# Optimization experiments

Measured on AMD Instinct MI355X. Metric: run time of the kernel, lower is better.

The kernel has to match this reference:

```python
import jax, jax.numpy as jnp
import numpy as np
from jax import lax

HIST_L = 8
HIST_AB = 64


def _hist2d(x1, nbin=HIST_AB):
    # channels 1 (a) and 2 (b); nonzero-masked weighted 2D histogram over [0,1]x[0,1]
    B = x1.shape[0]
    a = x1[:, 1].reshape(B, -1)
    b = x1[:, 2].reshape(B, -1)
    va = (a + 1.0) * 0.5
    vb = (b + 1.0) * 0.5
    w = ((a != 0) & (b != 0) & (va >= 0) & (va <= 1) & (vb >= 0) & (vb <= 1)).astype(jnp.float32)
    ia = jnp.clip(jnp.floor(va * nbin).astype(jnp.int32), 0, nbin - 1)
    ib = jnp.clip(jnp.floor(vb * nbin).astype(jnp.int32), 0, nbin - 1)
    idx = (jnp.arange(B, dtype=jnp.int32)[:, None] * (nbin * nbin) + ia * nbin + ib).reshape(-1)
    H = jax.ops.segment_sum(w.reshape(-1), idx, num_segments=B * nbin * nbin)
    H = H.reshape(B, nbin, nbin)
    H = H / jnp.sum(H, axis=(1, 2), keepdims=True)
    # np.rot90 followed by np.flip(axis=0) == transpose
    H = jnp.swapaxes(H, 1, 2)
    return H[:, None]  # [B,1,64,64]


def _hist1d(x1, nbin=HIST_L):
    # channel 0 (L); 1D histogram (second dummy dim has a single always-in-range bin)
    B = x1.shape[0]
    l = x1[:, 0].reshape(B, -1)
    v = (l + 1.0) * 0.5
    w = ((l != 0) & (v >= 0) & (v <= 1)).astype(jnp.float32)
    ib = jnp.clip(jnp.floor(v * nbin).astype(jnp.int32), 0, nbin - 1)
    idx = (jnp.arange(B, dtype=jnp.int32)[:, None] * nbin + ib).reshape(-1)
    H = jax.ops.segment_sum(w.reshape(-1), idx, num_segments=B * nbin).reshape(B, nbin)
    H = H / jnp.sum(H, axis=1, keepdims=True)
    return H[:, :, None, None]  # [B,8,1,1]


def _bn(x, g, b, m, v, eps=1e-5):
    inv = g * lax.rsqrt(v + eps)
    return x * inv[None, :, None, None] + (b - m * inv)[None, :, None, None]


def _hen(inp, w1, g1, b1, m1, v1, w2, g2, b2, m2, v2, wl, bl):
    dn = ('NCHW', 'OIHW', 'NCHW')
    # Conv 9->128, k1, pad 1 (grows 64 -> 66, matching torch padding=(1,1))
    y = lax.conv_general_dilated(inp, w1, (1, 1), [(1, 1), (1, 1)], dimension_numbers=dn)
    y = _bn(y, g1, b1, m1, v1)
    # MaxPool k3 s2 p1: 66 -> 33
    y = lax.reduce_window(y, -jnp.inf, lax.max, (1, 1, 3, 3), (1, 1, 2, 2),
                          [(0, 0), (0, 0), (1, 1), (1, 1)])
    y = jax.nn.relu(y)
    # Conv 128->1024, k3, pad 1
    y = lax.conv_general_dilated(y, w2, (1, 1), [(1, 1), (1, 1)], dimension_numbers=dn)
    y = jax.nn.relu(_bn(y, g2, b2, m2, v2))
    y = jnp.mean(y, axis=(2, 3))  # adaptive avg pool (1,1) -> [B,1024]
    return y @ wl.T + bl


def setup_inputs() -> dict:
    key = jax.random.key(0)
    ks = jax.random.split(key, 10)
    B, H, W = 16, 512, 512
    x = jax.random.normal(ks[0], (B, 2048), dtype=jnp.float32)
    x1 = jax.random.uniform(ks[1], (B, 3, H, W), dtype=jnp.float32)  # in [0,1) subset of [-1,1]
    w1 = jax.random.normal(ks[2], (128, 9, 1, 1), dtype=jnp.float32) * 0.1
    w2 = jax.random.normal(ks[3], (1024, 128, 3, 3), dtype=jnp.float32) * 0.02
    wl = jax.random.normal(ks[4], (256, 1024), dtype=jnp.float32) * 0.03
    bl = jax.random.normal(ks[5], (256,), dtype=jnp.float32) * 0.01
    g1 = jnp.ones((128,), jnp.float32); b1 = jnp.zeros((128,), jnp.float32)
    m1 = jnp.zeros((128,), jnp.float32); v1 = jnp.ones((128,), jnp.float32)
    g2 = jnp.ones((1024,), jnp.float32); b2 = jnp.zeros((1024,), jnp.float32)
    m2 = jnp.zeros((1024,), jnp.float32); v2 = jnp.ones((1024,), jnp.float32)
    return {"x": x, "x1": x1, "w1": w1, "g1": g1, "b1": b1, "m1": m1, "v1": v1,
            "w2": w2, "g2": g2, "b2": b2, "m2": m2, "v2": v2, "wl": wl, "bl": bl}


def reference(x, x1, w1, g1, b1, m1, v1, w2, g2, b2, m2, v2, wl, bl):
    hist_ab = _hist2d(x1)                                   # [B,1,64,64]
    hist_l = jnp.broadcast_to(_hist1d(x1), (x1.shape[0], HIST_L, HIST_AB, HIST_AB))
    hist_inp = jnp.concatenate([hist_ab, hist_l], axis=1)   # [B,9,64,64]
    h = _hen(hist_inp, w1, g1, b1, m1, v1, w2, g2, b2, m2, v2, wl, bl)  # [B,256]
    # NIMA.forward returns the concatenated features x (head/softmax output is discarded)
    return jnp.concatenate([x, h], axis=1)                  # [B,2304]
```

## Files before the change

kernel.cpp:

```cpp
#include <hip/hip_runtime.h>
#include <hip/hip_bf16.h>
#include <math.h>

typedef __attribute__((ext_vector_type(8))) short bf16x8;
typedef __attribute__((ext_vector_type(4))) float f32x4;
typedef __attribute__((ext_vector_type(8))) int i32x8;

#define HW 262144
#define M_SP 1089

#define OFF_CNT1P 0
#define OFF_HAB   2048
#define OFF_HL    67584
#define OFF_W2R   68096
#define OFF_ZT    362(0+1008)
#undef OFF_ZT
#define OFF_ZT    363008
#define OFF_FEATP 1026048
#define OFF_PART  1173504

__device__ inline unsigned wred_u32(unsigned v) {
#pragma unroll
    for (int off = 32; off > 0; off >>= 1) v += __shfl_down(v, off);
    return v;
}

__device__ inline unsigned char f2e4m3(float x) {
    unsigned s = (__float_as_uint(x) >> 31) << 7;
    float a = fabsf(x);
    if (a >= 464.f) return (unsigned char)(s | 0x7E);
    if (a < 0.0009765625f) return (unsigned char)s;
    int e; float m = frexpf(a, &e); (void)m;
    int E = e + 6;
    if (E >= 1) {
        float f = ldexpf(a, -(e - 1));
        int q = (int)rintf((f - 1.f) * 8.f);
        if (q == 8) { q = 0; ++E; }
        if (E >= 16) return (unsigned char)(s | 0x7E);
        return (unsigned char)(s | (E << 3) | q);
    } else {
        int q = (int)rintf(ldexpf(a, 9));
        if (q >= 8) return (unsigned char)(s | 0x08);
        return (unsigned char)(s | q);
    }
}

__global__ __launch_bounds__(512) void prep_kernel(const float* __restrict__ x1,
                                                   const float* __restrict__ w2,
                                                   unsigned* __restrict__ part,
                                                   unsigned* __restrict__ cnt1p,
                                                   unsigned char* __restrict__ w2r) {
    const int bid = blockIdx.x;
    const int tid = threadIdx.x;

    if (bid >= 256) {
        const int oc = (bid - 256) * 4 + (tid >> 7);
        const int ic = tid & 127;
        const float* src = w2 + oc * 1152 + ic * 9;
        float t[9];
#pragma unroll
        for (int k = 0; k < 9; ++k) t[k] = src[k];
#pragma unroll
        for (int k = 0; k < 9; ++k)
            w2r[(k << 17) + (oc << 7) + ic] = f2e4m3(t[k]);
        return;
    }

    const int b = bid >> 4, chunk = bid & 15;
    __shared__ unsigned h2[4096];
    __shared__ unsigned wv[8][8];
    for (int i = tid; i < 4096; i += 512) h2[i] = 0u;
    __syncthreads();

    const float4* L4 = (const float4*)(x1 + (size_t)b * 3 * HW);
    const float4* A4 = L4 + 65536;
    const float4* B4 = L4 + 131072;
    const int start = chunk * 4096;

    unsigned long long cL = 0ull;
#pragma unroll 1
    for (int it = 0; it < 8; it += 4) {
        float4 lb[4], ab[4], bbv[4];
#pragma unroll
        for (int u = 0; u < 4; ++u) {
            int idx = start + (it + u) * 512 + tid;
            lb[u] = L4[idx]; ab[u] = A4[idx]; bbv[u] = B4[idx];
        }
#pragma unroll
        for (int u = 0; u < 4; ++u) {
            const float lv[4] = {lb[u].x, lb[u].y, lb[u].z, lb[u].w};
            const float av[4] = {ab[u].x, ab[u].y, ab[u].z, ab[u].w};
            const float bv[4] = {bbv[u].x, bbv[u].y, bbv[u].z, bbv[u].w};
#pragma unroll
            for (int e = 0; e < 4; ++e) {
                float l = lv[e], a = av[e], bb = bv[e];
                float va = (a + 1.f) * 0.5f;
                float vb = (bb + 1.f) * 0.5f;
                if (a != 0.f && bb != 0.f && va >= 0.f && va <= 1.f && vb >= 0.f && vb <= 1.f) {
                    int ia = min(max((int)floorf(va * 64.f), 0), 63);
                    int ib = min(max((int)floorf(vb * 64.f), 0), 63);
                    atomicAdd(&h2[ia * 64 + ib], 1u);
                }
                float vl = (l + 1.f) * 0.5f;
                if (l != 0.f && vl >= 0.f && vl <= 1.f) {
                    int il = min(max((int)floorf(vl * 8.f), 0), 7);
                    cL += 1ull << (il << 3);
                }
            }
        }
    }
    unsigned cc[8];
#pragma unroll
    for (int e = 0; e < 8; ++e) cc[e] = (unsigned)((cL >> (e << 3)) & 0xffull);
#pragma unroll
    for (int e = 0; e < 8; ++e) cc[e] = wred_u32(cc[e]);
    if ((tid & 63) == 0) {
        int w = tid >> 6;
#pragma unroll
        for (int e = 0; e < 8; ++e) wv[w][e] = cc[e];
    }
    __syncthreads();
    if (tid < 8) {
        unsigned s = 0;
#pragma unroll
        for (int w = 0; w < 8; ++w) s += wv[w][tid];
        cnt1p[((size_t)b * 16 + chunk) * 8 + tid] = s;
    }
    uint4* pd = (uint4*)(part + (((size_t)b * 16 + chunk) << 12));
    const uint4* hs = (const uint4*)h2;
    for (int i = tid; i < 1024; i += 512) pd[i] = hs[i];
}

__global__ __launch_bounds__(256) void hist_norm(const unsigned* __restrict__ part,
                                                 const unsigned* __restrict__ cnt1p,
                                                 float* __restrict__ hab,
                                                 float* __restrict__ hl) {
    int b = blockIdx.x, tid = threadIdx.x;
    unsigned acc[16];
#pragma unroll
    for (int e = 0; e < 16; ++e) acc[e] = 0u;
#pragma unroll 1
    for (int k = 0; k < 16; ++k) {
        const uint4* p4 = (const uint4*)(part + (((size_t)b * 16 + k) << 12) + tid * 16);
#pragma unroll
        for (int u = 0; u < 4; ++u) {
            uint4 v = p4[u];
            acc[u*4+0] += v.x; acc[u*4+1] += v.y; acc[u*4+2] += v.z; acc[u*4+3] += v.w;
        }
    }
    unsigned ts = 0;
#pragma unroll
    for (int e = 0; e < 16; ++e) ts += acc[e];
    __shared__ float red[256];
    __shared__ float sc8[8];
    red[tid] = (float)ts;
    __syncthreads();
    for (int off = 128; off > 0; off >>= 1) {
        if (tid < off) red[tid] += red[tid + off];
        __syncthreads();
    }
    float inv2 = 1.f / red[0];
    int ia = tid >> 2, ibb = (tid & 3) << 4;
#pragma unroll
    for (int e = 0; e < 16; ++e)
        hab[(b << 12) + ((ibb + e) << 6) + ia] = (float)acc[e] * inv2;
    if (tid < 8) {
        unsigned sc = 0;
        for (int k = 0; k < 16; ++k) sc += cnt1p[((size_t)b * 16 + k) * 8 + tid];
        sc8[tid] = (float)sc;
    }
    __syncthreads();
    if (tid < 8) {
        float tt = 0.f;
#pragma unroll
        for (int c = 0; c < 8; ++c) tt += sc8[c];
        hl[b * 8 + tid] = sc8[tid] / tt;
    }
}

__global__ __launch_bounds__(256) void conv1_pool(
    const float* __restrict__ hab, const float* __restrict__ hl,
    const float* __restrict__ w1, const float* __restrict__ g1,
    const float* __restrict__ b1v, const float* __restrict__ m1,
    const float* __restrict__ v1, unsigned char* __restrict__ zt)
{
    const int p = blockIdx.x;
    const int b = blockIdx.y;
    __shared__ float aL[128], cL[128], sL[128];
    __shared__ float Hrow[3][64];
    __shared__ float qmx[33], qmn[33];
    __shared__ int qbd[33];
    const int tid = threadIdx.x;
    if (tid < 128) {
        int oc = tid;
        float inv = g1[oc] * rsqrtf(v1[oc] + 1e-5f);
        float s = b1v[oc] - m1[oc] * inv;
        float Kc = 0.f;
#pragma unroll
        for (int c = 1; c < 9; ++c) Kc = fmaf(w1[oc * 9 + c], hl[b * 8 + c - 1], Kc);
        aL[oc] = w1[oc * 9] * inv;
        cL[oc] = fmaf(Kc, inv, s);
        sL[oc] = s;
    }
    if (tid < 192) {
        int rr = tid >> 6, cc = tid & 63;
        int row = 2 * p - 2 + rr;
        Hrow[rr][cc] = (row >= 0 && row < 64) ? hab[b * 4096 + row * 64 + cc] : 0.f;
    }
    __syncthreads();
    if (tid < 33) {
        int q = tid;
        float mx = -1e30f, mn = 1e30f;
        int bd = 0;
#pragma unroll
        for (int dy = 0; dy < 3; ++dy) {
            int yi = 2 * p - 1 + dy;
            if (yi < 0 || yi > 65) continue;
#pragma unroll
            for (int dx = 0; dx < 3; ++dx) {
                int yj = 2 * q - 1 + dx;
                if (yj < 0 || yj > 65) continue;
                if (yi == 0 || yi == 65 || yj == 0 || yj == 65) bd = 1;
                else {
                    float h = Hrow[dy][2 * q - 2 + dx];
                    mx = fmaxf(mx, h); mn = fminf(mn, h);
                }
            }
        }
        qmx[q] = mx; qmn[q] = mn; qbd[q] = bd;
    }
    __syncthreads();
    unsigned char* zrow = zt + (((size_t)b * 37 + (p + 1)) * 35 + 1) * 128;
    for (int it = tid; it < 33 * 128; it += 256) {
        int q = it >> 7, oc = it & 127;
        float a = aL[oc];
        float v = fmaf(a, (a > 0.f ? qmx[q] : qmn[q]), cL[oc]);
        if (qbd[q]) v = fmaxf(v, sL[oc]);
        v = fmaxf(v, 0.f);
        zrow[q * 128 + oc] = f2e4m3(v);
    }
    {
        int col = (tid < 128) ? 0 : 34;
        int ch = tid & 127;
        zt[(((size_t)b * 37 + (p + 1)) * 35 + col) * 128 + ch] = 0;
    }
    if (p < 4) {
        int hr = (p == 0) ? 0 : (33 + p);
        unsigned char* hrow = zt + ((size_t)b * 37 + hr) * 35 * 128;
        for (int i = tid; i < 35 * 128; i += 256) hrow[i] = 0;
    }
}

__global__ __launch_bounds__(256, 2) void conv2_mfma(
        const unsigned char* __restrict__ zt,
        const unsigned char* __restrict__ w2r,
        const float* __restrict__ g2, const float* __restrict__ b2v,
        const float* __restrict__ m2, const float* __restrict__ v2,
        float* __restrict__ featp)
{
    __shared__ char lds[65536];
    const int tid = threadIdx.x;
    const int lane = tid & 63, wid = tid >> 6;
    const int b = blockIdx.z;
    const int nbase = blockIdx.x * 128;
    const int mbase = blockIdx.y * 128;
    const int lr16 = lane & 15, lk = lane >> 4;
    const int wm = (wid >> 1) * 64, wn = (wid & 1) * 64;

    const int csrc = ((lane & 7) ^ (lane >> 3)) << 4;
    const unsigned char* aS[4];
    const unsigned char* bS[4];
    {
        const unsigned char* ztb = zt + (size_t)b * 165760;
#pragma unroll
        for (int v = 0; v < 4; ++v) {
            int R = wid * 32 + v * 8 + (lane >> 3);
            int m = mbase + R;
            int p = m / 33, q = m - p * 33;
            aS[v] = ztb + (p * 35 + q) * 128 + csrc;
            bS[v] = w2r + (size_t)(nbase + R) * 128 + csrc;
        }
    }

    f32x4 acc[4][4];
#pragma unroll
    for (int i = 0; i < 4; ++i)
#pragma unroll
        for (int j = 0; j < 4; ++j) acc[i][j] = (f32x4){0.f, 0.f, 0.f, 0.f};

    auto stage = [&](int d, int tap) {
        const int kh = tap / 3, kw = tap - kh * 3;
        const int aoff = (kh * 35 + kw) * 128;
        const int boff = tap * 131072;
        char* ab = lds + d * 32768 + wid * 4096;
        char* bb = ab + 16384;
#pragma unroll
        for (int v = 0; v < 4; ++v)
            __builtin_amdgcn_global_load_lds(
                (const __attribute__((address_space(1))) unsigned int*)(aS[v] + aoff),
                (__attribute__((address_space(3))) unsigned int*)(ab + v * 1024), 16, 0, 0);
#pragma unroll
        for (int v = 0; v < 4; ++v)
            __builtin_amdgcn_global_load_lds(
                (const __attribute__((address_space(1))) unsigned int*)(bS[v] + boff),
                (__attribute__((address_space(3))) unsigned int*)(bb + v * 1024), 16, 0, 0);
    };

    auto compute = [&](int d) {
        const char* Ab = lds + d * 32768;
        const char* Bb = Ab + 16384;
        i32x8 af[4], bf[4];
#pragma unroll
        for (int i = 0; i < 4; ++i) {
            int row = wm + i * 16 + lr16;
            const char* base = Ab + row * 128;
            int x = row & 7;
            int4 lo = *(const int4*)(base + (((2 * lk) ^ x) << 4));
            int4 hi = *(const int4*)(base + (((2 * lk + 1) ^ x) << 4));
            af[i] = (i32x8){lo.x, lo.y, lo.z, lo.w, hi.x, hi.y, hi.z, hi.w};
        }
#pragma unroll
        for (int j = 0; j < 4; ++j) {
            int row = wn + j * 16 + lr16;
            const char* base = Bb + row * 128;
            int x = row & 7;
            int4 lo = *(const int4*)(base + (((2 * lk) ^ x) << 4));
            int4 hi = *(const int4*)(base + (((2 * lk + 1) ^ x) << 4));
            bf[j] = (i32x8){lo.x, lo.y, lo.z, lo.w, hi.x, hi.y, hi.z, hi.w};
        }
#pragma unroll
        for (int i = 0; i < 4; ++i)
#pragma unroll
            for (int j = 0; j < 4; ++j)
                acc[i][j] = __builtin_amdgcn_mfma_scale_f32_16x16x128_f8f6f4(
                    af[i], bf[j], acc[i][j],
                    0, 0,
                    0, 0x7F7F7F7F,
                    0, 0x7F7F7F7F);
    };

    stage(0, 0);
    __syncthreads();
#pragma unroll 1
    for (int s = 0; s < 9; ++s) {
        if (s < 8) stage((s + 1) & 1, s + 1);
        compute(s & 1);
        __syncthreads();
    }

    float* red = (float*)lds;
#pragma unroll
    for (int j = 0; j < 4; ++j) {
        int nl = wn + j * 16 + lr16;
        int n = nbase + nl;
        float inv = g2[n] * rsqrtf(v2[n] + 1e-5f);
        float sh = b2v[n] - m2[n] * inv;
        float ssum = 0.f;
#pragma unroll
        for (int i = 0; i < 4; ++i) {
            int mlb = wm + i * 16 + lk * 4;
#pragma unroll
            for (int r = 0; r < 4; ++r) {
                if (mbase + mlb + r < M_SP)
                    ssum += fmaxf(fmaf(acc[i][j][r], inv, sh), 0.f);
            }
        }
        red[((wid >> 1) * 4 + lk) * 128 + nl] = ssum;
    }
    __syncthreads();
    if (tid < 128) {
        float s = 0.f;
#pragma unroll
        for (int c = 0; c < 8; ++c) s += red[c * 128 + tid];
        featp[blockIdx.y * 16384 + b * 1024 + nbase + tid] = s * (1.f / 1089.f);
    }
}

__global__ __launch_bounds__(256) void linear_head(const float* __restrict__ featp,
                                                   const float* __restrict__ x,
                                                   const float* __restrict__ wl,
                                                   const float* __restrict__ bl,
                                                   float* __restrict__ out) {
    int jg = blockIdx.x, b = blockIdx.y;
    __shared__ float fsum[1024];
    int tid = threadIdx.x;
    if (tid < 128)
        out[b * 2304 + jg * 128 + tid] = x[b * 2048 + jg * 128 + tid];
    for (int c = tid; c < 1024; c += 256) {
        float s = 0.f;
#pragma unroll
        for (int mb = 0; mb < 9; ++mb) s += featp[mb * 16384 + b * 1024 + c];
        fsum[c] = s;
    }
    __syncthreads();
    int w = tid >> 6, lane = tid & 63;
#pragma unroll
    for (int jj = 0; jj < 4; ++jj) {
        int j = jg * 16 + w * 4 + jj;
        const float* wr = wl + j * 1024;
        float s = 0.f;
        for (int k = lane; k < 1024; k += 64) s = fmaf(fsum[k], wr[k], s);
#pragma unroll
        for (int off = 32; off > 0; off >>= 1) s += __shfl_down(s, off);
        if (lane == 0) out[b * 2304 + 2048 + j] = s + bl[j];
    }
}

extern "C" void kernel_launch(void* const* d_in, const int* in_sizes, int n_in,
                              void* d_out, int out_size, void* d_ws, size_t ws_size,
                              hipStream_t stream) {
    const float* x  = (const float*)d_in[0];
    const float* x1 = (const float*)d_in[1];
    const float* w1 = (const float*)d_in[2];
    const float* g1 = (const float*)d_in[3];
    const float* b1 = (const float*)d_in[4];
    const float* m1 = (const float*)d_in[5];
    const float* v1 = (const float*)d_in[6];
    const float* w2 = (const float*)d_in[7];
    const float* g2 = (const float*)d_in[8];
    const float* b2 = (const float*)d_in[9];
    const float* m2 = (const float*)d_in[10];
    const float* v2 = (const float*)d_in[11];
    const float* wl = (const float*)d_in[12];
    const float* bl = (const float*)d_in[13];
    float* out = (float*)d_out;

    float* wsf = (float*)d_ws;
    unsigned* cnt1p = (unsigned*)(wsf + OFF_CNT1P);
    float* hab   = wsf + OFF_HAB;
    float* hl    = wsf + OFF_HL;
    unsigned char* w2r = (unsigned char*)(wsf + OFF_W2R);
    unsigned char* zt  = (unsigned char*)(wsf + OFF_ZT);
    float* featp = wsf + OFF_FEATP;
    unsigned* part = (unsigned*)(wsf + OFF_PART);

    prep_kernel<<<512, 512, 0, stream>>>(x1, w2, part, cnt1p, w2r);
    hist_norm<<<16, 256, 0, stream>>>(part, cnt1p, hab, hl);
    conv1_pool<<<dim3(33, 16), 256, 0, stream>>>(hab, hl, w1, g1, b1, m1, v1, zt);
    conv2_mfma<<<dim3(8, 9, 16), 256, 0, stream>>>(zt, w2r, g2, b2, m2, v2, featp);
    linear_head<<<dim3(16, 16), 256, 0, stream>>>(featp, x, wl, bl, out);
}
```

Baseline: 83.72 us.

## Fuse histogram normalization into prep/conv1 and single-buffer conv2 for occupancy

Removes the hist_norm kernel. Each prep block now computes a partial total count, and conv1_pool reduces the 16 partial histograms for its three rows directly and normalizes them on the fly, which saves one launch and a round trip through global memory. conv2_mfma drops the LDS double buffer (64KB down to 32KB) and raises its launch-bounds occupancy hint from 2 to 5, waiting on each stage before compute. This trades the load/compute overlap inside a block for more resident blocks. conv1_pool also reads part with strided, uncoalesced accesses, repeated by each of the 33 row blocks.

```diff
diff --git a/kernel.cpp b/kernel.cpp
--- a/kernel.cpp
+++ b/kernel.cpp
@@ -2,22 +2,18 @@
 #include <hip/hip_bf16.h>
 #include <math.h>
 
-typedef __attribute__((ext_vector_type(8))) short bf16x8;
 typedef __attribute__((ext_vector_type(4))) float f32x4;
 typedef __attribute__((ext_vector_type(8))) int i32x8;
 
 #define HW 262144
 #define M_SP 1089
 
-#define OFF_CNT1P 0
-#define OFF_HAB   2048
-#define OFF_HL    67584
-#define OFF_W2R   68096
-#define OFF_ZT    362(0+1008)
-#undef OFF_ZT
-#define OFF_ZT    363008
-#define OFF_FEATP 1026048
-#define OFF_PART  1173504
+#define OFF_PART  0
+#define OFF_BSUM  1048576
+#define OFF_CNT1P 1048832
+#define OFF_W2R   1050880
+#define OFF_ZT    1345792
+#define OFF_FEATP 2008832
 
 __device__ inline unsigned wred_u32(unsigned v) {
 #pragma unroll
@@ -48,6 +44,7 @@
 __global__ __launch_bounds__(512) void prep_kernel(const float* __restrict__ x1,
                                                    const float* __restrict__ w2,
                                                    unsigned* __restrict__ part,
+                                                   unsigned* __restrict__ bsum,
                                                    unsigned* __restrict__ cnt1p,
                                                    unsigned char* __restrict__ w2r) {
     const int bid = blockIdx.x;
@@ -69,6 +66,7 @@
     const int b = bid >> 4, chunk = bid & 15;
     __shared__ unsigned h2[4096];
     __shared__ unsigned wv[8][8];
+    __shared__ unsigned rsum[512];
     for (int i = tid; i < 4096; i += 512) h2[i] = 0u;
     __syncthreads();
 
@@ -128,58 +126,24 @@
     }
     uint4* pd = (uint4*)(part + (((size_t)b * 16 + chunk) << 12));
     const uint4* hs = (const uint4*)h2;
-    for (int i = tid; i < 1024; i += 512) pd[i] = hs[i];
-}
-
-__global__ __launch_bounds__(256) void hist_norm(const unsigned* __restrict__ part,
-                                                 const unsigned* __restrict__ cnt1p,
-                                                 float* __restrict__ hab,
-                                                 float* __restrict__ hl) {
-    int b = blockIdx.x, tid = threadIdx.x;
-    unsigned acc[16];
-#pragma unroll
-    for (int e = 0; e < 16; ++e) acc[e] = 0u;
-#pragma unroll 1
-    for (int k = 0; k < 16; ++k) {
-        const uint4* p4 = (const uint4*)(part + (((size_t)b * 16 + k) << 12) + tid * 16);
-#pragma unroll
-        for (int u = 0; u < 4; ++u) {
-            uint4 v = p4[u];
-            acc[u*4+0] += v.x; acc[u*4+1] += v.y; acc[u*4+2] += v.z; acc[u*4+3] += v.w;
-        }
-    }
-    unsigned ts = 0;
-#pragma unroll
-    for (int e = 0; e < 16; ++e) ts += acc[e];
-    __shared__ float red[256];
-    __shared__ float sc8[8];
-    red[tid] = (float)ts;
-    __syncthreads();
-    for (int off = 128; off > 0; off >>= 1) {
-        if (tid < off) red[tid] += red[tid + off];
+    unsigned mysum = 0;
+    for (int i = tid; i < 1024; i += 512) {
+        uint4 v = hs[i];
+        pd[i] = v;
+        mysum += v.x + v.y + v.z + v.w;
+    }
+    rsum[tid] = mysum;
+    __syncthreads();
+    for (int off = 256; off > 0; off >>= 1) {
+        if (tid < off) rsum[tid] += rsum[tid + off];
         __syncthreads();
     }
-    float inv2 = 1.f / red[0];
-    int ia = tid >> 2, ibb = (tid & 3) << 4;
-#pragma unroll
-    for (int e = 0; e < 16; ++e)
-        hab[(b << 12) + ((ibb + e) << 6) + ia] = (float)acc[e] * inv2;
-    if (tid < 8) {
-        unsigned sc = 0;
-        for (int k = 0; k < 16; ++k) sc += cnt1p[((size_t)b * 16 + k) * 8 + tid];
-        sc8[tid] = (float)sc;
-    }
-    __syncthreads();
-    if (tid < 8) {
-        float tt = 0.f;
-#pragma unroll
-        for (int c = 0; c < 8; ++c) tt += sc8[c];
-        hl[b * 8 + tid] = sc8[tid] / tt;
-    }
+    if (tid == 0) bsum[b * 16 + chunk] = rsum[0];
 }
 
 __global__ __launch_bounds__(256) void conv1_pool(
-    const float* __restrict__ hab, const float* __restrict__ hl,
+    const unsigned* __restrict__ part, const unsigned* __restrict__ bsum,
+    const unsigned* __restrict__ cnt1p,
     const float* __restrict__ w1, const float* __restrict__ g1,
     const float* __restrict__ b1v, const float* __restrict__ m1,
     const float* __restrict__ v1, unsigned char* __restrict__ zt)
@@ -188,28 +152,57 @@
     const int b = blockIdx.y;
     __shared__ float aL[128], cL[128], sL[128];
     __shared__ float Hrow[3][64];
+    __shared__ unsigned bs16[16];
+    __shared__ float hlsh[8];
     __shared__ float qmx[33], qmn[33];
     __shared__ int qbd[33];
     const int tid = threadIdx.x;
+
+    if (tid < 192) {
+        int rr = tid >> 6, cc = tid & 63;
+        int row = 2 * p - 2 + rr;
+        float s = 0.f;
+        if (row >= 0 && row < 64) {
+            unsigned acc = 0;
+#pragma unroll 1
+            for (int k = 0; k < 16; ++k)
+                acc += part[(((size_t)b * 16 + k) << 12) + (cc << 6) + row];
+            s = (float)acc;
+        }
+        Hrow[rr][cc] = s;
+    } else if (tid < 208) {
+        bs16[tid - 192] = bsum[b * 16 + (tid - 192)];
+    } else if (tid < 216) {
+        int c = tid - 208;
+        unsigned s = 0;
+#pragma unroll 1
+        for (int k = 0; k < 16; ++k) s += cnt1p[((size_t)b * 16 + k) * 8 + c];
+        hlsh[c] = (float)s;
+    }
+    __syncthreads();
+
+    unsigned tt = 0;
+#pragma unroll
+    for (int i = 0; i < 16; ++i) tt += bs16[i];
+    const float inv2 = 1.f / (float)tt;
+    float hltot = 0.f;
+#pragma unroll
+    for (int c = 0; c < 8; ++c) hltot += hlsh[c];
+    const float invl = 1.f / hltot;
+
     if (tid < 128) {
         int oc = tid;
         float inv = g1[oc] * rsqrtf(v1[oc] + 1e-5f);
         float s = b1v[oc] - m1[oc] * inv;
         float Kc = 0.f;
 #pragma unroll
-        for (int c = 1; c < 9; ++c) Kc = fmaf(w1[oc * 9 + c], hl[b * 8 + c - 1], Kc);
+        for (int c = 1; c < 9; ++c) Kc = fmaf(w1[oc * 9 + c], hlsh[c - 1] * invl, Kc);
         aL[oc] = w1[oc * 9] * inv;
         cL[oc] = fmaf(Kc, inv, s);
         sL[oc] = s;
     }
-    if (tid < 192) {
-        int rr = tid >> 6, cc = tid & 63;
-        int row = 2 * p - 2 + rr;
-        Hrow[rr][cc] = (row >= 0 && row < 64) ? hab[b * 4096 + row * 64 + cc] : 0.f;
-    }
-    __syncthreads();
-    if (tid < 33) {
-        int q = tid;
+    if (tid >= 128 && tid < 161) {
+        int q = tid - 128;
         float mx = -1e30f, mn = 1e30f;
         int bd = 0;
 #pragma unroll
@@ -227,7 +220,7 @@
                 }
             }
         }
-        qmx[q] = mx; qmn[q] = mn; qbd[q] = bd;
+        qmx[q] = mx * inv2; qmn[q] = mn * inv2; qbd[q] = bd;
     }
     __syncthreads();
     unsigned char* zrow = zt + (((size_t)b * 37 + (p + 1)) * 35 + 1) * 128;
@@ -251,14 +244,14 @@
     }
 }
 
-__global__ __launch_bounds__(256, 2) void conv2_mfma(
+__global__ __launch_bounds__(256, 5) void conv2_mfma(
         const unsigned char* __restrict__ zt,
         const unsigned char* __restrict__ w2r,
         const float* __restrict__ g2, const float* __restrict__ b2v,
         const float* __restrict__ m2, const float* __restrict__ v2,
         float* __restrict__ featp)
 {
-    __shared__ char lds[65536];
+    __shared__ char lds[32768];
     const int tid = threadIdx.x;
     const int lane = tid & 63, wid = tid >> 6;
     const int b = blockIdx.z;
@@ -288,12 +281,12 @@
 #pragma unroll
         for (int j = 0; j < 4; ++j) acc[i][j] = (f32x4){0.f, 0.f, 0.f, 0.f};
 
-    auto stage = [&](int d, int tap) {
+    auto stage = [&](int tap) {
         const int kh = tap / 3, kw = tap - kh * 3;
         const int aoff = (kh * 35 + kw) * 128;
         const int boff = tap * 131072;
-        char* ab = lds + d * 32768 + wid * 4096;
-        char* bb = ab + 16384;
+        char* ab = lds + wid * 4096;
+        char* bb = lds + 16384 + wid * 4096;
 #pragma unroll
         for (int v = 0; v < 4; ++v)
             __builtin_amdgcn_global_load_lds(
@@ -306,9 +299,9 @@
                 (__attribute__((address_space(3))) unsigned int*)(bb + v * 1024), 16, 0, 0);
     };
 
-    auto compute = [&](int d) {
-        const char* Ab = lds + d * 32768;
-        const char* Bb = Ab + 16384;
+    auto compute = [&]() {
+        const char* Ab = lds;
+        const char* Bb = lds + 16384;
         i32x8 af[4], bf[4];
 #pragma unroll
         for (int i = 0; i < 4; ++i) {
@@ -334,17 +327,15 @@
             for (int j = 0; j < 4; ++j)
                 acc[i][j] = __builtin_amdgcn_mfma_scale_f32_16x16x128_f8f6f4(
                     af[i], bf[j], acc[i][j],
-                    0, 0,
-                    0, 0x7F7F7F7F,
-                    0, 0x7F7F7F7F);
+                    0, 0, 0, 0x7F7F7F7F, 0, 0x7F7F7F7F);
     };
 
-    stage(0, 0);
-    __syncthreads();
 #pragma unroll 1
-    for (int s = 0; s < 9; ++s) {
-        if (s < 8) stage((s + 1) & 1, s + 1);
-        compute(s & 1);
+    for (int t = 0; t < 9; ++t) {
+        stage(t);
+        asm volatile("s_waitcnt vmcnt(0)" ::: "memory");
+        __syncthreads();
+        compute();
         __syncthreads();
     }
 
@@ -426,17 +417,15 @@
     float* out = (float*)d_out;
 
     float* wsf = (float*)d_ws;
+    unsigned* part  = (unsigned*)(wsf + OFF_PART);
+    unsigned* bsum  = (unsigned*)(wsf + OFF_BSUM);
     unsigned* cnt1p = (unsigned*)(wsf + OFF_CNT1P);
-    float* hab   = wsf + OFF_HAB;
-    float* hl    = wsf + OFF_HL;
     unsigned char* w2r = (unsigned char*)(wsf + OFF_W2R);
     unsigned char* zt  = (unsigned char*)(wsf + OFF_ZT);
     float* featp = wsf + OFF_FEATP;
-    unsigned* part = (unsigned*)(wsf + OFF_PART);
-
-    prep_kernel<<<512, 512, 0, stream>>>(x1, w2, part, cnt1p, w2r);
-    hist_norm<<<16, 256, 0, stream>>>(part, cnt1p, hab, hl);
-    conv1_pool<<<dim3(33, 16), 256, 0, stream>>>(hab, hl, w1, g1, b1, m1, v1, zt);
+
+    prep_kernel<<<512, 512, 0, stream>>>(x1, w2, part, bsum, cnt1p, w2r);
+    conv1_pool<<<dim3(33, 16), 256, 0, stream>>>(part, bsum, cnt1p, w1, g1, b1, m1, v1, zt);
     conv2_mfma<<<dim3(8, 9, 16), 256, 0, stream>>>(zt, w2r, g2, b2, m2, v2, featp);
     linear_head<<<dim3(16, 16), 256, 0, stream>>>(featp, x, wl, bl, out);
 }
```

Result: slower. 191.3 us (+128.6%).
